# Kernel optimization log

Measured on AMD Instinct MI355X. Metric: run time of the kernel, lower is better.

Reference implementation:

```python
import jax, jax.numpy as jnp
import numpy as np

B, H, W, C = 4, 128, 128, 256
HEADS, DHEAD = 8, 32


def conv2d(x, w, b=None, groups=1, pad=0):
    # x: [N,C,H,W], w: [O, C//groups, kh, kw]
    out = jax.lax.conv_general_dilated(
        x, w, window_strides=(1, 1), padding=[(pad, pad), (pad, pad)],
        dimension_numbers=("NCHW", "OIHW", "NCHW"), feature_group_count=groups)
    if b is not None:
        out = out + b[None, :, None, None]
    return out


def setup_inputs() -> dict:
    key = jax.random.key(0)
    ks = jax.random.split(key, 16)
    g = lambda i, shape, s=0.02: jax.random.normal(ks[i], shape, jnp.float32) * s
    return {
        "x": jax.random.normal(ks[0], (B, H, W, C), jnp.float32),
        "mask": jax.random.uniform(ks[1], (1, C, H, W), jnp.float32),
        "wq": g(2, (C, C)),
        "wk": g(3, (C, C)),
        "wv": g(4, (C, C)),
        "rescale": jnp.ones((HEADS, 1, 1), jnp.float32),
        "wproj": g(5, (C, C)),
        "bproj": jnp.zeros((C,), jnp.float32),
        "mg_w1": g(6, (C, C, 1, 1)),
        "mg_b1": jnp.zeros((C,), jnp.float32),
        "mg_w2": g(7, (C, C, 1, 1)),
        "mg_b2": jnp.zeros((C,), jnp.float32),
        "mg_dw": g(8, (C, 1, 5, 5)),
        "mg_db": jnp.zeros((C,), jnp.float32),
        "be_w1": g(9, (C, 1, 3, 3)),
        "be_w2": g(10, (C, 1, 3, 3)),
    }


def _l2norm(t, axis):
    n = jnp.sqrt(jnp.sum(t * t, axis=axis, keepdims=True))
    return t / jnp.maximum(n, 1e-12)


def reference(x, mask, wq, wk, wv, rescale, wproj, bproj,
              mg_w1, mg_b1, mg_w2, mg_b2, mg_dw, mg_db, be_w1, be_w2):
    b, h, w, c = x.shape
    heads = rescale.shape[0]
    d = c // heads
    n = h * w

    xf = x.reshape(b, n, c)
    q_inp = xf @ wq   # [b,n,c]
    k_inp = xf @ wk
    v_inp = xf @ wv

    # MaskGuidedMechanism (h==w so shift_back is identity)
    m = conv2d(mask, mg_w1, mg_b1)                                   # [1,c,h,w]
    attn_map = jax.nn.sigmoid(conv2d(conv2d(m, mg_w2, mg_b2), mg_dw, mg_db, groups=c, pad=2))
    m = m * attn_map + m
    mask_emb = jnp.transpose(m, (0, 2, 3, 1))                        # [1,h,w,c]
    ma = jnp.broadcast_to(mask_emb, (b, h, w, c)).reshape(b, n, c)

    split = lambda t: t.reshape(b, n, heads, d).transpose(0, 2, 1, 3)  # [b,heads,n,d]
    q, k, v, ma = map(split, (q_inp, k_inp, v_inp, ma))
    v = v * ma

    # channel attention: normalize over token dim n
    qn = _l2norm(q, axis=2)
    kn = _l2norm(k, axis=2)
    attn = jnp.einsum("bhni,bhnj->bhij", kn, qn)                     # [b,heads,d,d]
    attn = jax.nn.softmax(attn * rescale, axis=-1)
    out = jnp.einsum("bhij,bhnj->bhin", attn, v)                     # [b,heads,d,n]

    out = out.transpose(0, 3, 1, 2).reshape(b, n, heads * d)         # [b,n,c]
    out_c = (out @ wproj + bproj).reshape(b, h, w, c)

    # band_emb: depthwise3x3 -> GELU(exact) -> depthwise3x3 on v_inp image
    v_img = v_inp.reshape(b, h, w, c).transpose(0, 3, 1, 2)          # [b,c,h,w]
    y = conv2d(v_img, be_w1, groups=c, pad=1)
    y = jax.nn.gelu(y, approximate=False)
    y = conv2d(y, be_w2, groups=c, pad=1)
    out_p = y.transpose(0, 2, 3, 1)

    return out_c + out_p
```

## Files before the change

### kernel.cpp

```cpp
#include <hip/hip_runtime.h>
#include <stdint.h>

#define B 4
#define HW 128
#define C 256
#define NTOK 16384
#define MALL 65536
#define HEADS 8
#define DH 32

typedef float f32x4 __attribute__((ext_vector_type(4)));
typedef short s16x8 __attribute__((ext_vector_type(8)));
typedef short s16x4 __attribute__((ext_vector_type(4)));
typedef __bf16 bf16x8 __attribute__((ext_vector_type(8)));

__device__ __forceinline__ float bf2f(unsigned short u) {
  union { unsigned int i; float f; } x;
  x.i = ((unsigned int)u) << 16;
  return x.f;
}
__device__ __forceinline__ unsigned short f2bf(float f) {
  union { float f; unsigned int i; } x;
  x.f = f;
  unsigned int lsb = (x.i >> 16) & 1u;
  unsigned int r = x.i + 0x7fffu + lsb;
  return (unsigned short)(r >> 16);
}

__device__ __forceinline__ void gload_lds16(const void* g, void* l) {
  auto gp = reinterpret_cast<const __attribute__((address_space(1))) unsigned int*>(
      reinterpret_cast<uintptr_t>(g));
  auto lp = reinterpret_cast<__attribute__((address_space(3))) unsigned int*>(
      reinterpret_cast<uintptr_t>(l));
  __builtin_amdgcn_global_load_lds(gp, lp, 16, 0, 0);
}

#define CFENCE asm volatile("" ::: "memory")
#define RAWBAR()                      \
  do {                                \
    CFENCE;                           \
    __builtin_amdgcn_s_barrier();     \
    CFENCE;                           \
  } while (0)

__global__ __launch_bounds__(256) void cast_x_kernel(const float* __restrict__ x,
                                                     unsigned short* __restrict__ xb) {
  const size_t stride = (size_t)gridDim.x * blockDim.x * 4;
  for (size_t i = ((size_t)blockIdx.x * blockDim.x + threadIdx.x) * 4; i < (size_t)MALL * C;
       i += stride) {
    const float4 v = *(const float4*)&x[i];
    s16x4 o;
    o[0] = (short)f2bf(v.x);
    o[1] = (short)f2bf(v.y);
    o[2] = (short)f2bf(v.z);
    o[3] = (short)f2bf(v.w);
    *(s16x4*)&xb[i] = o;
  }
}

__global__ __launch_bounds__(256) void prep_w_kernel(
    const float* __restrict__ wq, const float* __restrict__ wk, const float* __restrict__ wv,
    const float* __restrict__ wproj, const float* __restrict__ w1, const float* __restrict__ w2,
    unsigned short* __restrict__ wqkvT, unsigned short* __restrict__ wprojT,
    unsigned short* __restrict__ w1b, unsigned short* __restrict__ w2b) {
  const int idx = blockIdx.x * 256 + threadIdx.x;
  const int mat = blockIdx.y;
  const int n = idx >> 8, k = idx & 255;
  switch (mat) {
    case 0: wqkvT[idx] = f2bf(wq[k * 256 + n]); break;
    case 1: wqkvT[65536 + idx] = f2bf(wk[k * 256 + n]); break;
    case 2: wqkvT[131072 + idx] = f2bf(wv[k * 256 + n]); break;
    case 3: wprojT[idx] = f2bf(wproj[k * 256 + n]); break;
    case 4: w1b[idx] = f2bf(w1[idx]); break;
    case 5: w2b[idx] = f2bf(w2[idx]); break;
  }
}

__global__ __launch_bounds__(1024) void tmask_kernel(const float* __restrict__ mask,
                                                     unsigned short* __restrict__ mT) {
  __shared__ float tile[32][33];
  const int p0 = blockIdx.x * 32, c0 = blockIdx.y * 32;
  const int tx = threadIdx.x & 31, ty = threadIdx.x >> 5;
  tile[ty][tx] = mask[(size_t)(c0 + ty) * NTOK + p0 + tx];
  __syncthreads();
  mT[(size_t)(p0 + ty) * C + c0 + tx] = f2bf(tile[tx][ty]);
}

__global__ __launch_bounds__(512) void gemm_bt256_kernel(
    const unsigned short* __restrict__ A, const unsigned short* __restrict__ Bt,
    const int nbn, const int mode, unsigned short* __restrict__ ob0,
    unsigned short* __restrict__ ob1, unsigned short* __restrict__ ob2,
    const float* __restrict__ bias, float* __restrict__ of32) {
  __shared__ unsigned short lA[3][8192];
  __shared__ unsigned short lB[3][8192];
  const int nwg = gridDim.x;
  const int bid = blockIdx.x;
  const int qd = nwg >> 3, rr = nwg & 7;
  const int xcd = bid & 7, sidx = bid >> 3;
  const int swz = (xcd < rr ? xcd * (qd + 1) : rr * (qd + 1) + (xcd - rr) * qd) + sidx;
  const int m0 = (swz / nbn) * 256;
  const int n0 = (swz % nbn) * 256;
  const int t = threadIdx.x;
  const int w = t >> 6, l = t & 63;
  const int wr = w >> 2, wc = w & 3;
  const int lr = l & 15, lg = l >> 4;

  const int srow = t >> 2;
  const int ssl = (t & 3) ^ ((t >> 3) & 3);

  auto stageA = [&](int kt) {
    unsigned short* d = &lA[kt % 3][0];
    const size_t kb = ((size_t)kt * 32 + ssl * 8) * 2;
    gload_lds16((const char*)A + ((size_t)(m0 + srow) * 256) * 2 + kb, (char*)d + t * 16);
    gload_lds16((const char*)A + ((size_t)(m0 + 128 + srow) * 256) * 2 + kb,
                (char*)d + 8192 + t * 16);
  };
  auto stageB = [&](int kt) {
    unsigned short* d = &lB[kt % 3][0];
    const size_t kb = ((size_t)kt * 32 + ssl * 8) * 2;
    gload_lds16((const char*)Bt + ((size_t)(n0 + srow) * 256) * 2 + kb, (char*)d + t * 16);
    gload_lds16((const char*)Bt + ((size_t)(n0 + 128 + srow) * 256) * 2 + kb,
                (char*)d + 8192 + t * 16);
  };

  f32x4 acc[8][4];
#pragma unroll
  for (int m = 0; m < 8; ++m)
#pragma unroll
    for (int j = 0; j < 4; ++j) acc[m][j] = f32x4{0.f, 0.f, 0.f, 0.f};

  const int asl = (lg ^ ((lr >> 1) & 3)) * 8;
  const int aoff = wr * 4096 + lr * 32 + asl;
  const int boff = (wc >> 1) * 4096 + ((wc & 1) * 64 + lr) * 32 + asl;

  stageA(0); stageB(0); stageA(1); stageB(1);
  asm volatile("s_waitcnt vmcnt(4)" ::: "memory");
  RAWBAR();

#pragma unroll
  for (int kt = 0; kt < 8; ++kt) {
    const int buf = kt % 3;
    bf16x8 bfr[4], af[4];
#pragma unroll
    for (int j = 0; j < 4; ++j) bfr[j] = *(const bf16x8*)&lB[buf][boff + j * 512];
#pragma unroll
    for (int m = 0; m < 4; ++m) af[m] = *(const bf16x8*)&lA[buf][aoff + m * 512];
    if (kt < 6) stageA(kt + 2);
    RAWBAR();
    __builtin_amdgcn_s_setprio(1);
#pragma unroll
    for (int m = 0; m < 4; ++m)
#pragma unroll
      for (int j = 0; j < 4; ++j)
        acc[m][j] = __builtin_amdgcn_mfma_f32_16x16x32_bf16(af[m], bfr[j], acc[m][j], 0, 0, 0);
    __builtin_amdgcn_s_setprio(0);
    RAWBAR();
#pragma unroll
    for (int m = 0; m < 4; ++m) af[m] = *(const bf16x8*)&lA[buf][aoff + (m + 4) * 512];
    if (kt < 6) stageB(kt + 2);
    RAWBAR();
    __builtin_amdgcn_s_setprio(1);
#pragma unroll
    for (int m = 0; m < 4; ++m)
#pragma unroll
      for (int j = 0; j < 4; ++j)
        acc[m + 4][j] =
            __builtin_amdgcn_mfma_f32_16x16x32_bf16(af[m], bfr[j], acc[m + 4][j], 0, 0, 0);
    __builtin_amdgcn_s_setprio(0);
    if (kt < 6) asm volatile("s_waitcnt vmcnt(4)" ::: "memory");
    else asm volatile("s_waitcnt vmcnt(0)" ::: "memory");
    RAWBAR();
  }

#pragma unroll
  for (int m = 0; m < 8; ++m) {
    const int grow = m0 + wr * 128 + m * 16 + lg * 4;
#pragma unroll
    for (int j = 0; j < 4; ++j) {
      const int gcol = n0 + wc * 64 + j * 16 + lr;
#pragma unroll
      for (int r = 0; r < 4; ++r) {
        const float v = acc[m][j][r];
        const size_t row = (size_t)(grow + r);
        if (mode == 0) {
          unsigned short* dst = (n0 < 256) ? ob0 : (n0 < 512 ? ob1 : ob2);
          dst[row * C + (gcol & 255)] = f2bf(v);
        } else {
          const size_t idx = row * C + gcol;
          of32[idx] += v + bias[gcol];
        }
      }
    }
  }
}

__global__ __launch_bounds__(256) void gemm_bt_kernel(
    const unsigned short* __restrict__ A, const unsigned short* __restrict__ Bt, const int K,
    const int nbn, const int mode, unsigned short* __restrict__ ob0,
    unsigned short* __restrict__ ob1, unsigned short* __restrict__ ob2,
    const float* __restrict__ bias, float* __restrict__ of32) {
  __shared__ unsigned short lA[2][128 * 64];
  __shared__ unsigned short lB[2][128 * 64];
  const int nwg = gridDim.x;
  const int bid = blockIdx.x;
  const int qd = nwg >> 3, rr = nwg & 7;
  const int xcd = bid & 7, sidx = bid >> 3;
  const int swz = (xcd < rr ? xcd * (qd + 1) : rr * (qd + 1) + (xcd - rr) * qd) + sidx;
  const int m0 = (swz / nbn) * 128;
  const int n0 = (swz % nbn) * 128;
  const int t = threadIdx.x;
  const int w = t >> 6, l = t & 63;
  const int wr = w >> 1, wc = w & 1;
  const int lr = l & 15, lg = l >> 4;

  const int strow = (l >> 3);
  const int scolb = (((l & 7) ^ strow) << 4);

  f32x4 acc[4][4];
#pragma unroll
  for (int i = 0; i < 4; ++i)
#pragma unroll
    for (int j = 0; j < 4; ++j) acc[i][j] = f32x4{0.f, 0.f, 0.f, 0.f};

  auto stage = [&](int buf, int k0) {
#pragma unroll
    for (int s = 0; s < 4; ++s) {
      const int seg = w * 4 + s;
      const int row = seg * 8 + strow;
      gload_lds16((const char*)A + ((size_t)(m0 + row) * K + k0) * 2 + scolb,
                  (char*)&lA[buf][0] + seg * 1024 + (l & 7) * 16);
      gload_lds16((const char*)Bt + ((size_t)(n0 + row) * K + k0) * 2 + scolb,
                  (char*)&lB[buf][0] + seg * 1024 + (l & 7) * 16);
    }
  };
  auto compute = [&](int buf) {
#pragma unroll
    for (int kk = 0; kk < 64; kk += 32) {
      bf16x8 af[4], bfr[4];
      const int sbase = (kk >> 3) + lg;
      const int p = (sbase ^ (lr & 7)) << 3;
#pragma unroll
      for (int i = 0; i < 4; ++i)
        af[i] = *(const bf16x8*)&lA[buf][(wr * 64 + i * 16 + lr) * 64 + p];
#pragma unroll
      for (int j = 0; j < 4; ++j)
        bfr[j] = *(const bf16x8*)&lB[buf][(wc * 64 + j * 16 + lr) * 64 + p];
#pragma unroll
      for (int i = 0; i < 4; ++i)
#pragma unroll
        for (int j = 0; j < 4; ++j)
          acc[i][j] = __builtin_amdgcn_mfma_f32_16x16x32_bf16(af[i], bfr[j], acc[i][j], 0, 0, 0);
    }
  };

  stage(0, 0);
  __syncthreads();
  int cur = 0;
  for (int k0 = 64; k0 < K; k0 += 64) {
    stage(cur ^ 1, k0);
    compute(cur);
    __syncthreads();
    cur ^= 1;
  }
  compute(cur);

#pragma unroll
  for (int i = 0; i < 4; ++i) {
    const int grow = m0 + wr * 64 + i * 16 + lg * 4;
#pragma unroll
    for (int j = 0; j < 4; ++j) {
      const int gcol = n0 + wc * 64 + j * 16 + lr;
#pragma unroll
      for (int r = 0; r < 4; ++r) {
        const float v = acc[i][j][r];
        const size_t row = (size_t)(grow + r);
        if (mode == 0) {
          unsigned short* dst = (gcol < 256) ? ob0 : (gcol < 512 ? ob1 : ob2);
          dst[row * C + (gcol & 255)] = f2bf(v);
        } else if (mode == 1) {
          ob0[row * C + gcol] = f2bf(v + bias[gcol]);
        } else {
          const size_t idx = row * C + gcol;
          of32[idx] += v + bias[gcol];
        }
      }
    }
  }
}

__global__ __launch_bounds__(256) void mask_dw5_kernel(
    const unsigned short* __restrict__ m2, const unsigned short* __restrict__ m1,
    const float* __restrict__ dw, const float* __restrict__ db,
    unsigned short* __restrict__ memb) {
  __shared__ float wlds[25 * 256];
  __shared__ float blds[256];
  const int t = threadIdx.x;
  const int y = blockIdx.y;
  const int x0 = blockIdx.x * 16 + (t >> 6) * 4;
  const int cg = (t & 63) * 4;
#pragma unroll
  for (int e = 0; e < 25; ++e) wlds[e * 256 + t] = dw[t * 25 + e];
  blds[t] = db[t];
  __syncthreads();

  const f32x4 bias = *(const f32x4*)&blds[cg];
  f32x4 acc[4];
#pragma unroll
  for (int xi = 0; xi < 4; ++xi) acc[xi] = bias;

#pragma unroll
  for (int dy = 0; dy < 5; ++dy) {
    const int yy = y + dy - 2;
    if (yy < 0 || yy >= HW) continue;
    f32x4 col[8];
#pragma unroll
    for (int j = 0; j < 8; ++j) {
      const int xx = x0 - 2 + j;
      if (xx >= 0 && xx < HW) {
        const s16x4 v = *(const s16x4*)&m2[((size_t)yy * HW + xx) * C + cg];
        col[j][0] = bf2f((unsigned short)v[0]);
        col[j][1] = bf2f((unsigned short)v[1]);
        col[j][2] = bf2f((unsigned short)v[2]);
        col[j][3] = bf2f((unsigned short)v[3]);
      } else {
        col[j] = f32x4{0.f, 0.f, 0.f, 0.f};
      }
    }
#pragma unroll
    for (int dx = 0; dx < 5; ++dx) {
      const f32x4 wv = *(const f32x4*)&wlds[(dy * 5 + dx) * 256 + cg];
#pragma unroll
      for (int xi = 0; xi < 4; ++xi) acc[xi] += wv * col[dx + xi];
    }
  }

#pragma unroll
  for (int xi = 0; xi < 4; ++xi) {
    const size_t oi = ((size_t)y * HW + x0 + xi) * C + cg;
    const s16x4 mv = *(const s16x4*)&m1[oi];
    s16x4 o;
#pragma unroll
    for (int ch = 0; ch < 4; ++ch) {
      const float a = 1.f / (1.f + __expf(-acc[xi][ch]));
      o[ch] = (short)f2bf(bf2f((unsigned short)mv[ch]) * (1.f + a));
    }
    *(s16x4*)&memb[oi] = o;
  }
}

__global__ __launch_bounds__(256) void gram_kernel(const unsigned short* __restrict__ qb,
                                                   const unsigned short* __restrict__ kb,
                                                   float* __restrict__ Gpart,
                                                   float* __restrict__ ssq,
                                                   float* __restrict__ ssk) {
  const int chunk = blockIdx.x;
  const int h = blockIdx.y;
  const int b = blockIdx.z;
  __shared__ unsigned short lk[128 * 32], lq[128 * 32];
  const int t = threadIdx.x;
  const int wv = t >> 6;
  const int i0 = (t & 7) * 4, j0 = ((t >> 3) & 7) * 4;
  const int lrow = t >> 2, lcb = (t & 3) * 8;
  float acc[4][4] = {};
  float sq[8] = {}, sk[8] = {};
  for (int sub = 0; sub < 8; ++sub) {
    const size_t nbase = (size_t)b * NTOK + chunk * 1024 + sub * 128;
    __syncthreads();
#pragma unroll
    for (int it = 0; it < 2; ++it) {
      const int row = it * 64 + lrow;
      const s16x8 kv8 = *(const s16x8*)&kb[(nbase + row) * C + h * 32 + lcb];
      const s16x8 qv8 = *(const s16x8*)&qb[(nbase + row) * C + h * 32 + lcb];
      *(s16x8*)&lk[row * 32 + lcb] = kv8;
      *(s16x8*)&lq[row * 32 + lcb] = qv8;
#pragma unroll
      for (int e = 0; e < 8; ++e) {
        const float kf = bf2f((unsigned short)kv8[e]);
        sk[e] += kf * kf;
        const float qf = bf2f((unsigned short)qv8[e]);
        sq[e] += qf * qf;
      }
    }
    __syncthreads();
    for (int n = wv; n < 128; n += 4) {
      s16x4 kv = *(const s16x4*)&lk[n * 32 + i0];
      s16x4 qv = *(const s16x4*)&lq[n * 32 + j0];
      float kf[4], qf[4];
#pragma unroll
      for (int e = 0; e < 4; ++e) {
        kf[e] = bf2f((unsigned short)kv[e]);
        qf[e] = bf2f((unsigned short)qv[e]);
      }
#pragma unroll
      for (int a = 0; a < 4; ++a)
#pragma unroll
        for (int bb = 0; bb < 4; ++bb) acc[a][bb] += kf[a] * qf[bb];
    }
  }
  const int pc = chunk * 4 + wv;
  float* dst = Gpart + (((size_t)pc * B + b) * HEADS + h) * 1024;
#pragma unroll
  for (int a = 0; a < 4; ++a)
#pragma unroll
    for (int bb = 0; bb < 4; ++bb) dst[(i0 + a) * 32 + (j0 + bb)] = acc[a][bb];
  __syncthreads();
  float* fq = (float*)lq;
  float* fk = (float*)lk;
#pragma unroll
  for (int e = 0; e < 8; ++e) {
    fq[t * 8 + e] = sq[e];
    fk[t * 8 + e] = sk[e];
  }
  __syncthreads();
  if (t < 32) {
    const int tm = t >> 3, e = t & 7;
    float s1 = 0.f, s2 = 0.f;
    for (int k2 = 0; k2 < 64; ++k2) {
      const int tt = tm + k2 * 4;
      s1 += fq[tt * 8 + e];
      s2 += fk[tt * 8 + e];
    }
    ssq[((size_t)b * 16 + chunk) * C + h * 32 + t] = s1;
    ssk[((size_t)b * 16 + chunk) * C + h * 32 + t] = s2;
  }
}

__global__ __launch_bounds__(256) void softmax_kernel(
    const float* __restrict__ Gpart, const float* __restrict__ ssq,
    const float* __restrict__ ssk, const float* __restrict__ rescale,
    unsigned short* __restrict__ attnb) {
  const int h = blockIdx.x, b = blockIdx.y;
  const int t = threadIdx.x;
  __shared__ float G[1024];
  __shared__ float nq[32], nk[32];
#pragma unroll
  for (int e = 0; e < 4; ++e) {
    const int cell = e * 256 + t;
    float s = 0.f;
    for (int pc = 0; pc < 64; ++pc)
      s += Gpart[(((size_t)pc * B + b) * HEADS + h) * 1024 + cell];
    G[cell] = s;
  }
  if (t < 64) {
    const int d = t & 31;
    const float* ss = (t < 32) ? ssq : ssk;
    float s = 0.f;
    for (int ch = 0; ch < 16; ++ch) s += ss[((size_t)b * 16 + ch) * C + h * 32 + d];
    const float nn = fmaxf(sqrtf(s), 1e-12f);
    if (t < 32) nq[d] = nn;
    else nk[d] = nn;
  }
  __syncthreads();
  if (t < 32) {
    const int i = t;
    const float rs = rescale[h];
    float row[32];
    float mx = -1e30f;
#pragma unroll
    for (int j = 0; j < 32; ++j) {
      const float v = G[i * 32 + j] / (nk[i] * nq[j]) * rs;
      row[j] = v;
      mx = fmaxf(mx, v);
    }
    float sum = 0.f;
#pragma unroll
    for (int j = 0; j < 32; ++j) {
      const float e = expf(row[j] - mx);
      row[j] = e;
      sum += e;
    }
    const float inv = 1.f / sum;
#pragma unroll
    for (int j = 0; j < 32; ++j)
      attnb[(((size_t)b * HEADS + h) * 32 + i) * 32 + j] = f2bf(row[j] * inv);
  }
}

#define PVP 264
#define ATP 40
__global__ __launch_bounds__(256) void pv_kernel(const unsigned short* __restrict__ vb,
                                                 const unsigned short* __restrict__ memb,
                                                 const unsigned short* __restrict__ attnb,
                                                 unsigned short* __restrict__ outp) {
  const int n0 = blockIdx.x * 64;
  const int b = blockIdx.y;
  __shared__ unsigned short vma[64 * PVP];
  __shared__ unsigned short at[HEADS * 32 * ATP];
  const int t = threadIdx.x, w = t >> 6, l = t & 63;
  const int lr = l & 15, lg = l >> 4;
  for (int e = t; e < 8192; e += 256) {
    const int h = e >> 10, ij = e & 1023;
    at[(h * 32 + (ij >> 5)) * ATP + (ij & 31)] = attnb[(size_t)b * 8192 + e];
  }
  {
    const int row = t >> 2, cs = (t & 3) * 64;
#pragma unroll
    for (int i2 = 0; i2 < 8; ++i2) {
      const int c = cs + i2 * 8;
      s16x8 vv = *(const s16x8*)&vb[((size_t)b * NTOK + n0 + row) * C + c];
      s16x8 mm = *(const s16x8*)&memb[(size_t)(n0 + row) * C + c];
      s16x8 o;
#pragma unroll
      for (int e = 0; e < 8; ++e)
        o[e] = (short)f2bf(bf2f((unsigned short)vv[e]) * bf2f((unsigned short)mm[e]));
      *(s16x8*)&vma[row * PVP + c] = o;
    }
  }
  __syncthreads();
  f32x4 acc[4][4];
#pragma unroll
  for (int i = 0; i < 4; ++i)
#pragma unroll
    for (int j = 0; j < 4; ++j) acc[i][j] = f32x4{0.f, 0.f, 0.f, 0.f};
#pragma unroll
  for (int j = 0; j < 4; ++j) {
    const int head = w * 2 + (j >> 1);
    const int colh = (j & 1) * 16 + lr;
    const bf16x8 bfr = *(const bf16x8*)&at[(head * 32 + colh) * ATP + lg * 8];
#pragma unroll
    for (int i = 0; i < 4; ++i) {
      const bf16x8 af = *(const bf16x8*)&vma[(i * 16 + lr) * PVP + head * 32 + lg * 8];
      acc[i][j] = __builtin_amdgcn_mfma_f32_16x16x32_bf16(af, bfr, acc[i][j], 0, 0, 0);
    }
  }
#pragma unroll
  for (int i = 0; i < 4; ++i) {
#pragma unroll
    for (int j = 0; j < 4; ++j) {
      const int head = w * 2 + (j >> 1);
      const int gcol = head * 32 + (j & 1) * 16 + lr;
      const int grow = n0 + i * 16 + lg * 4;
#pragma unroll
      for (int r = 0; r < 4; ++r)
        outp[((size_t)b * NTOK + grow + r) * C + gcol] = f2bf(acc[i][j][r]);
    }
  }
}

__global__ __launch_bounds__(512) void dw3_kernel(const unsigned short* __restrict__ in,
                                                  const float* __restrict__ wgt,
                                                  unsigned short* __restrict__ out_bf,
                                                  float* __restrict__ out_f32,
                                                  const int do_gelu, const int write_f32) {
  const int y = blockIdx.x;
  const int b = blockIdx.y;
  const int t = threadIdx.x;
  const int cg = (t & 63) * 4;
  const int x0 = (t >> 6) * 16;
  float w[9][4];
#pragma unroll
  for (int e = 0; e < 9; ++e)
#pragma unroll
    for (int ch = 0; ch < 4; ++ch) w[e][ch] = wgt[(cg + ch) * 9 + e];
  const int ym = y - 1, yp = y + 1;
  const bool hm = (ym >= 0), hp = (yp < HW);
  const size_t base = (size_t)b * NTOK * C + cg;
  auto ld4 = [&](int yy, int xx) -> f32x4 {
    const s16x4 v = *(const s16x4*)&in[base + ((size_t)yy * HW + xx) * C];
    f32x4 f;
    f[0] = bf2f((unsigned short)v[0]);
    f[1] = bf2f((unsigned short)v[1]);
    f[2] = bf2f((unsigned short)v[2]);
    f[3] = bf2f((unsigned short)v[3]);
    return f;
  };
  const f32x4 zero = {0.f, 0.f, 0.f, 0.f};
  f32x4 a0, a1, a2, b0, b1, b2;
  if (x0 > 0) {
    a0 = hm ? ld4(ym, x0 - 1) : zero;
    a1 = ld4(y, x0 - 1);
    a2 = hp ? ld4(yp, x0 - 1) : zero;
  } else {
    a0 = a1 = a2 = zero;
  }
  b0 = hm ? ld4(ym, x0) : zero;
  b1 = ld4(y, x0);
  b2 = hp ? ld4(yp, x0) : zero;
  for (int xi = 0; xi < 16; ++xi) {
    const int x = x0 + xi;
    f32x4 c0, c1, c2;
    if (x + 1 < HW) {
      c0 = hm ? ld4(ym, x + 1) : zero;
      c1 = ld4(y, x + 1);
      c2 = hp ? ld4(yp, x + 1) : zero;
    } else {
      c0 = c1 = c2 = zero;
    }
    float res[4];
#pragma unroll
    for (int ch = 0; ch < 4; ++ch) {
      float r = w[0][ch] * a0[ch] + w[1][ch] * b0[ch] + w[2][ch] * c0[ch] +
                w[3][ch] * a1[ch] + w[4][ch] * b1[ch] + w[5][ch] * c1[ch] +
                w[6][ch] * a2[ch] + w[7][ch] * b2[ch] + w[8][ch] * c2[ch];
      if (do_gelu) r = 0.5f * r * (1.f + erff(r * 0.70710678118654752f));
      res[ch] = r;
    }
    const size_t oi = base + ((size_t)y * HW + x) * C;
    if (write_f32) {
      const f32x4 o = {res[0], res[1], res[2], res[3]};
      *(f32x4*)&out_f32[oi] = o;
    } else {
      s16x4 o;
      o[0] = (short)f2bf(res[0]);
      o[1] = (short)f2bf(res[1]);
      o[2] = (short)f2bf(res[2]);
      o[3] = (short)f2bf(res[3]);
      *(s16x4*)&out_bf[oi] = o;
    }
    a0 = b0; a1 = b1; a2 = b2;
    b0 = c0; b1 = c1; b2 = c2;
  }
}

extern "C" void kernel_launch(void* const* d_in, const int* in_sizes, int n_in, void* d_out,
                              int out_size, void* d_ws, size_t ws_size, hipStream_t stream) {
  (void)in_sizes; (void)n_in; (void)out_size; (void)ws_size;
  const float* x = (const float*)d_in[0];
  const float* maskp = (const float*)d_in[1];
  const float* wq = (const float*)d_in[2];
  const float* wk = (const float*)d_in[3];
  const float* wv = (const float*)d_in[4];
  const float* rescale = (const float*)d_in[5];
  const float* wproj = (const float*)d_in[6];
  const float* bproj = (const float*)d_in[7];
  const float* mg_w1 = (const float*)d_in[8];
  const float* mg_b1 = (const float*)d_in[9];
  const float* mg_w2 = (const float*)d_in[10];
  const float* mg_b2 = (const float*)d_in[11];
  const float* mg_dw = (const float*)d_in[12];
  const float* mg_db = (const float*)d_in[13];
  const float* be_w1 = (const float*)d_in[14];
  const float* be_w2 = (const float*)d_in[15];
  float* out = (float*)d_out;
  char* ws = (char*)d_ws;

  unsigned short* xb = (unsigned short*)(ws + 0ull);
  unsigned short* qb = (unsigned short*)(ws + 33554432ull);
  unsigned short* kb = (unsigned short*)(ws + 67108864ull);
  unsigned short* vb = (unsigned short*)(ws + 100663296ull);
  unsigned short* mT = (unsigned short*)(ws + 134217728ull);
  unsigned short* m1b = (unsigned short*)(ws + 142606336ull);
  unsigned short* m2b = (unsigned short*)(ws + 150994944ull);
  unsigned short* wqkvT = (unsigned short*)(ws + 159383552ull);
  unsigned short* wprojT = (unsigned short*)(ws + 159776768ull);
  unsigned short* w1b = (unsigned short*)(ws + 159907840ull);
  unsigned short* w2b = (unsigned short*)(ws + 160038912ull);
  float* ssq = (float*)(ws + 160169984ull);
  float* ssk = (float*)(ws + 160432128ull);
  unsigned short* attnb = (unsigned short*)(ws + 160694272ull);
  float* Gpart = (float*)m2b;
  unsigned short* memb = mT;
  unsigned short* outpre = xb;
  unsigned short* y1 = qb;

  cast_x_kernel<<<2048, 256, 0, stream>>>(x, xb);
  prep_w_kernel<<<dim3(256, 6), 256, 0, stream>>>(wq, wk, wv, wproj, mg_w1, mg_w2, wqkvT,
                                                  wprojT, w1b, w2b);
  tmask_kernel<<<dim3(512, 8), 1024, 0, stream>>>(maskp, mT);
  gemm_bt_kernel<<<256, 256, 0, stream>>>(mT, w1b, 256, 2, 1, m1b, nullptr, nullptr, mg_b1,
                                          nullptr);
  gemm_bt_kernel<<<256, 256, 0, stream>>>(m1b, w2b, 256, 2, 1, m2b, nullptr, nullptr, mg_b2,
                                          nullptr);
  mask_dw5_kernel<<<dim3(8, 128), 256, 0, stream>>>(m2b, m1b, mg_dw, mg_db, memb);
  gemm_bt256_kernel<<<768, 512, 0, stream>>>(xb, wqkvT, 3, 0, qb, kb, vb, nullptr, nullptr);
  gram_kernel<<<dim3(16, 8, 4), 256, 0, stream>>>(qb, kb, Gpart, ssq, ssk);
  softmax_kernel<<<dim3(8, 4), 256, 0, stream>>>(Gpart, ssq, ssk, rescale, attnb);
  pv_kernel<<<dim3(256, 4), 256, 0, stream>>>(vb, memb, attnb, outpre);
  dw3_kernel<<<dim3(128, 4), 512, 0, stream>>>(vb, be_w1, y1, nullptr, 1, 0);
  dw3_kernel<<<dim3(128, 4), 512, 0, stream>>>(y1, be_w2, nullptr, out, 0, 1);
  gemm_bt256_kernel<<<256, 512, 0, stream>>>(outpre, wprojT, 1, 2, nullptr, nullptr, nullptr,
                                             bproj, out);
}
```

Measured before the change: 327.2 us.

## Stage GEMM epilogue through LDS for coalesced stores and fuse band-emb add

The 256x256 GEMM epilogue now writes accumulators into padded LDS (reusing the staging buffers) and then emits row-contiguous 16-byte vector stores, instead of scattered per-element stores. The second depthwise conv now writes a bf16 intermediate (y2) rather than accumulating fp32 into the output. The projection GEMM reads y2 and writes out = acc + bias + y2 directly, which removes the read-modify-write of the fp32 output. This adds extra LDS barriers and round trips in the epilogue, and y2 is stored in bf16, which may slightly change precision.

```diff
diff --git a/kernel.cpp b/kernel.cpp
--- a/kernel.cpp
+++ b/kernel.cpp
@@ -41,6 +41,12 @@
     CFENCE;                           \
     __builtin_amdgcn_s_barrier();     \
     CFENCE;                           \
+  } while (0)
+#define LDSBAR()                                        \
+  do {                                                  \
+    asm volatile("s_waitcnt lgkmcnt(0)" ::: "memory");  \
+    __builtin_amdgcn_s_barrier();                       \
+    CFENCE;                                             \
   } while (0)
 
 __global__ __launch_bounds__(256) void cast_x_kernel(const float* __restrict__ x,
@@ -90,9 +96,11 @@
     const unsigned short* __restrict__ A, const unsigned short* __restrict__ Bt,
     const int nbn, const int mode, unsigned short* __restrict__ ob0,
     unsigned short* __restrict__ ob1, unsigned short* __restrict__ ob2,
-    const float* __restrict__ bias, float* __restrict__ of32) {
-  __shared__ unsigned short lA[3][8192];
-  __shared__ unsigned short lB[3][8192];
+    const float* __restrict__ bias, float* __restrict__ of32,
+    const unsigned short* __restrict__ y2) {
+  __shared__ unsigned short smem[49152];
+  unsigned short* lAb = smem;
+  unsigned short* lBb = smem + 24576;
   const int nwg = gridDim.x;
   const int bid = blockIdx.x;
   const int qd = nwg >> 3, rr = nwg & 7;
@@ -109,14 +117,14 @@
   const int ssl = (t & 3) ^ ((t >> 3) & 3);
 
   auto stageA = [&](int kt) {
-    unsigned short* d = &lA[kt % 3][0];
+    unsigned short* d = lAb + (kt % 3) * 8192;
     const size_t kb = ((size_t)kt * 32 + ssl * 8) * 2;
     gload_lds16((const char*)A + ((size_t)(m0 + srow) * 256) * 2 + kb, (char*)d + t * 16);
     gload_lds16((const char*)A + ((size_t)(m0 + 128 + srow) * 256) * 2 + kb,
                 (char*)d + 8192 + t * 16);
   };
   auto stageB = [&](int kt) {
-    unsigned short* d = &lB[kt % 3][0];
+    unsigned short* d = lBb + (kt % 3) * 8192;
     const size_t kb = ((size_t)kt * 32 + ssl * 8) * 2;
     gload_lds16((const char*)Bt + ((size_t)(n0 + srow) * 256) * 2 + kb, (char*)d + t * 16);
     gload_lds16((const char*)Bt + ((size_t)(n0 + 128 + srow) * 256) * 2 + kb,
@@ -130,7 +138,8 @@
     for (int j = 0; j < 4; ++j) acc[m][j] = f32x4{0.f, 0.f, 0.f, 0.f};
 
   const int asl = (lg ^ ((lr >> 1) & 3)) * 8;
-  const int aoff = wr * 4096 + lr * 32 + asl;
+  const int aoff = lr * 32 + asl;
+  const int awb = wr * 4096;
   const int boff = (wc >> 1) * 4096 + ((wc & 1) * 64 + lr) * 32 + asl;
 
   stageA(0); stageB(0); stageA(1); stageB(1);
@@ -139,12 +148,13 @@
 
 #pragma unroll
   for (int kt = 0; kt < 8; ++kt) {
-    const int buf = kt % 3;
+    const unsigned short* bufA = lAb + (kt % 3) * 8192;
+    const unsigned short* bufB = lBb + (kt % 3) * 8192;
     bf16x8 bfr[4], af[4];
 #pragma unroll
-    for (int j = 0; j < 4; ++j) bfr[j] = *(const bf16x8*)&lB[buf][boff + j * 512];
-#pragma unroll
-    for (int m = 0; m < 4; ++m) af[m] = *(const bf16x8*)&lA[buf][aoff + m * 512];
+    for (int j = 0; j < 4; ++j) bfr[j] = *(const bf16x8*)&bufB[boff + j * 512];
+#pragma unroll
+    for (int m = 0; m < 4; ++m) af[m] = *(const bf16x8*)&bufA[awb + aoff + m * 512];
     if (kt < 6) stageA(kt + 2);
     RAWBAR();
     __builtin_amdgcn_s_setprio(1);
@@ -156,7 +166,7 @@
     __builtin_amdgcn_s_setprio(0);
     RAWBAR();
 #pragma unroll
-    for (int m = 0; m < 4; ++m) af[m] = *(const bf16x8*)&lA[buf][aoff + (m + 4) * 512];
+    for (int m = 0; m < 4; ++m) af[m] = *(const bf16x8*)&bufA[awb + aoff + (m + 4) * 512];
     if (kt < 6) stageB(kt + 2);
     RAWBAR();
     __builtin_amdgcn_s_setprio(1);
@@ -172,23 +182,62 @@
     RAWBAR();
   }
 
-#pragma unroll
-  for (int m = 0; m < 8; ++m) {
-    const int grow = m0 + wr * 128 + m * 16 + lg * 4;
-#pragma unroll
-    for (int j = 0; j < 4; ++j) {
-      const int gcol = n0 + wc * 64 + j * 16 + lr;
-#pragma unroll
-      for (int r = 0; r < 4; ++r) {
-        const float v = acc[m][j][r];
-        const size_t row = (size_t)(grow + r);
-        if (mode == 0) {
-          unsigned short* dst = (n0 < 256) ? ob0 : (n0 < 512 ? ob1 : ob2);
-          dst[row * C + (gcol & 255)] = f2bf(v);
-        } else {
-          const size_t idx = row * C + gcol;
-          of32[idx] += v + bias[gcol];
+  if (mode == 0) {
+    unsigned short* dst = (n0 < 256) ? ob0 : (n0 < 512 ? ob1 : ob2);
+    unsigned short* eph = smem;
+#pragma unroll
+    for (int h = 0; h < 2; ++h) {
+      LDSBAR();
+#pragma unroll
+      for (int mm = 0; mm < 4; ++mm) {
+        const int m = h * 4 + mm;
+        const int lrow = wr * 64 + mm * 16 + lg * 4;
+#pragma unroll
+        for (int j = 0; j < 4; ++j) {
+          const int col = wc * 64 + j * 16 + lr;
+#pragma unroll
+          for (int r = 0; r < 4; ++r) eph[(lrow + r) * 264 + col] = f2bf(acc[m][j][r]);
         }
+      }
+      LDSBAR();
+      const int col16 = t & 31;
+#pragma unroll
+      for (int c2 = 0; c2 < 8; ++c2) {
+        const int lrow = c2 * 16 + (t >> 5);
+        const int grow = m0 + (lrow >> 6) * 128 + h * 64 + (lrow & 63);
+        const s16x8 v = *(const s16x8*)&eph[lrow * 264 + col16 * 8];
+        *(s16x8*)&dst[(size_t)grow * C + col16 * 8] = v;
+      }
+    }
+  } else {
+    float* ephf = (float*)smem;
+    const int colc = t & 63;
+    const f32x4 bv = *(const f32x4*)&bias[colc * 4];
+#pragma unroll
+    for (int qtr = 0; qtr < 4; ++qtr) {
+      LDSBAR();
+#pragma unroll
+      for (int mm = 0; mm < 2; ++mm) {
+        const int m = qtr * 2 + mm;
+        const int lrow = wr * 32 + mm * 16 + lg * 4;
+#pragma unroll
+        for (int j = 0; j < 4; ++j) {
+          const int col = wc * 64 + j * 16 + lr;
+#pragma unroll
+          for (int r = 0; r < 4; ++r) ephf[(lrow + r) * 260 + col] = acc[m][j][r];
+        }
+      }
+      LDSBAR();
+#pragma unroll
+      for (int c2 = 0; c2 < 8; ++c2) {
+        const int lrow = c2 * 8 + (t >> 6);
+        const int grow = m0 + (lrow >> 5) * 128 + qtr * 32 + (lrow & 31);
+        const f32x4 v = *(const f32x4*)&ephf[lrow * 260 + colc * 4];
+        const s16x4 yv = *(const s16x4*)&y2[(size_t)grow * C + colc * 4];
+        f32x4 o;
+#pragma unroll
+        for (int e = 0; e < 4; ++e) o[e] = v[e] + bv[e] + bf2f((unsigned short)yv[e]);
+        *(f32x4*)&of32[(size_t)grow * C + colc * 4] = o;
       }
     }
   }
@@ -652,6 +701,7 @@
   unsigned short* memb = mT;
   unsigned short* outpre = xb;
   unsigned short* y1 = qb;
+  unsigned short* y2 = kb;
 
   cast_x_kernel<<<2048, 256, 0, stream>>>(x, xb);
   prep_w_kernel<<<dim3(256, 6), 256, 0, stream>>>(wq, wk, wv, wproj, mg_w1, mg_w2, wqkvT,
@@ -662,12 +712,13 @@
   gemm_bt_kernel<<<256, 256, 0, stream>>>(m1b, w2b, 256, 2, 1, m2b, nullptr, nullptr, mg_b2,
                                           nullptr);
   mask_dw5_kernel<<<dim3(8, 128), 256, 0, stream>>>(m2b, m1b, mg_dw, mg_db, memb);
-  gemm_bt256_kernel<<<768, 512, 0, stream>>>(xb, wqkvT, 3, 0, qb, kb, vb, nullptr, nullptr);
+  gemm_bt256_kernel<<<768, 512, 0, stream>>>(xb, wqkvT, 3, 0, qb, kb, vb, nullptr, nullptr,
+                                             nullptr);
   gram_kernel<<<dim3(16, 8, 4), 256, 0, stream>>>(qb, kb, Gpart, ssq, ssk);
   softmax_kernel<<<dim3(8, 4), 256, 0, stream>>>(Gpart, ssq, ssk, rescale, attnb);
   pv_kernel<<<dim3(256, 4), 256, 0, stream>>>(vb, memb, attnb, outpre);
   dw3_kernel<<<dim3(128, 4), 512, 0, stream>>>(vb, be_w1, y1, nullptr, 1, 0);
-  dw3_kernel<<<dim3(128, 4), 512, 0, stream>>>(y1, be_w2, nullptr, out, 0, 1);
+  dw3_kernel<<<dim3(128, 4), 512, 0, stream>>>(y1, be_w2, y2, nullptr, 0, 0);
   gemm_bt256_kernel<<<256, 512, 0, stream>>>(outpre, wprojT, 1, 2, nullptr, nullptr, nullptr,
-                                             bproj, out);
-}
+                                             bproj, out, y2);
+}
```

After: 299.6 us. 1.09x faster.
